# Kernel tuning notes

Hardware: AMD Instinct MI355X
Metric: run time of the kernel (lower is better)

## Reference

```python
import jax, jax.numpy as jnp
import numpy as np

B, L, D = 16, 1024, 512
EPS = 1e-6


def setup_inputs() -> dict:
    key = jax.random.key(0)
    ks = jax.random.split(key, 12)
    inp = {
        'q': jax.random.normal(ks[0], (B, L, D), jnp.float32),
        'k': jax.random.normal(ks[1], (B, L, D), jnp.float32),
        'v': jax.random.normal(ks[2], (B, L, D), jnp.float32),
        'inputs_lengths': jax.random.randint(ks[3], (B,), 1, L + 1),
        'distance_matrix': jax.random.uniform(ks[4], (B, L, L), jnp.float32),
        'Wq': jax.random.normal(ks[5], (D, D), jnp.float32) / np.sqrt(D),
        'Wk': jax.random.normal(ks[6], (D, D), jnp.float32) / np.sqrt(D),
        'Wv': jax.random.normal(ks[7], (D, D), jnp.float32) / np.sqrt(D),
        'Wqt': jax.random.normal(ks[8], (D, D), jnp.float32) / np.sqrt(D),
        'Wkt': jax.random.normal(ks[9], (D, D), jnp.float32) / np.sqrt(D),
        'Wfc': jax.random.normal(ks[10], (D, D), jnp.float32) / np.sqrt(D),
        'gamma': jnp.ones((D,), jnp.float32),
        'beta': jnp.zeros((D,), jnp.float32),
    }
    return inp


def reference(q, k, v, inputs_lengths, distance_matrix, Wq, Wk, Wv, Wqt, Wkt, Wfc, gamma, beta):
    temperature = jnp.asarray(D, q.dtype) ** 0.5
    residual = q
    # projections (torch Linear: x @ W.T)
    qp = jnp.einsum('bld,ed->ble', q, Wq)
    kp = jnp.einsum('bld,ed->ble', k, Wk)
    vp = jnp.einsum('bld,ed->ble', v, Wv)
    qt = jnp.einsum('bld,ed->ble', q, Wqt)
    kt = jnp.einsum('bld,ed->ble', k, Wkt)
    # distance-weighted time features: [B,L,L] @ [B,L,D]
    qt = jnp.einsum('blm,bmd->bld', distance_matrix, qt)
    kt = jnp.einsum('blm,bmd->bld', distance_matrix, kt)
    # scores: content + distance term
    attn = jnp.einsum('bld,bmd->blm', qp / temperature, kp)
    attn = attn + jnp.einsum('bld,bmd->blm', qt / temperature, kt)
    # pad_zero_masking: zero out key positions beyond each sequence length
    mask = (jnp.arange(L)[None, :] < inputs_lengths[:, None]).astype(attn.dtype)  # [B, L]
    mask = mask[:, None, :]  # [B, 1, L] broadcast over query dim
    attn = jnp.tanh(attn * mask) * mask
    out = jnp.einsum('blm,bmd->bld', attn, vp)
    out = jnp.einsum('bld,ed->ble', out, Wfc) + residual
    # LayerNorm(eps=1e-6)
    mu = jnp.mean(out, axis=-1, keepdims=True)
    var = jnp.mean((out - mu) ** 2, axis=-1, keepdims=True)
    out = (out - mu) * jax.lax.rsqrt(var + EPS) * gamma + beta
    return (out, attn)
```

## Files before the change

kernel.cpp:

```cpp
#include <hip/hip_runtime.h>
#include <math.h>

#define LL 1024
#define DD 512
#define NB 16

typedef __attribute__((ext_vector_type(8))) short bf16x8;
typedef __attribute__((ext_vector_type(4))) float f32x4;
typedef unsigned short u16;
typedef unsigned int u32;
typedef const __attribute__((address_space(1))) void* gptr_t;
typedef __attribute__((address_space(3))) void* sptr_t;

static const long NLD = (long)NB * LL * DD;
static const long NLL = (long)NB * LL * LL;

__device__ __forceinline__ u16 f2bf(float x) {
  u32 u = __float_as_uint(x);
  u += 0x7fffu + ((u >> 16) & 1u);
  return (u16)(u >> 16);
}
__device__ __forceinline__ float bf2f(u16 h) {
  return __uint_as_float((u32)h << 16);
}
// ... 60 lines not shown
    u16* __restrict__ Wq_h, u16* __restrict__ Wk_h, u16* __restrict__ Wv_h,
    u16* __restrict__ Wfc_h, u16* __restrict__ Wqt_h,
    u16* __restrict__ Wqt_l, u16* __restrict__ Wkt_h,
    u16* __restrict__ Wkt_l) {
  const int z = blockIdx.z;
  const float* x;
  u16 *hi, *lo = nullptr;
  switch (z) {
    case 0: x = Wq; hi = Wq_h; break;
    case 1: x = Wk; hi = Wk_h; break;
    case 2: x = Wv; hi = Wv_h; break;
    case 3: x = Wfc; hi = Wfc_h; break;
    case 4: x = Wqt; hi = Wqt_h; lo = Wqt_l; break;
    default: x = Wkt; hi = Wkt_h; lo = Wkt_l; break;
  }
  const long i = ((long)blockIdx.x * 256 + threadIdx.x) * 4;
  const float4 v = *(const float4*)(x + i);
  ushort4 h;
  h.x = f2bf(v.x);
  h.y = f2bf(v.y);
  h.z = f2bf(v.z);
  h.w = f2bf(v.w);
  *(ushort4*)(hi + i) = h;
  if (z >= 4) {
    ushort4 s;
    s.x = f2bf(v.x - bf2f(h.x));
    s.y = f2bf(v.y - bf2f(h.y));
    s.z = f2bf(v.z - bf2f(h.z));
    s.w = f2bf(v.w - bf2f(h.w));
    *(ushort4*)(lo + i) = s;
  }
}

template <int NISS>
__device__ __forceinline__ void stage_tile(const u16* __restrict__ G, long ld,
                                           int row0, int k0, char* lds, int w,
                                           int l) {
#pragma unroll
  for (int i = 0; i < NISS; ++i) {
    const int off = i * 4096 + w * 1024 + l * 16;
    const int r = off >> 6;
    const int cp = (off >> 4) & 3;
    const int c = cp ^ ((r >> 1) & 3);
    __builtin_amdgcn_global_load_lds(
        (gptr_t)(G + (long)(row0 + r) * ld + k0 + c * 8),
        (sptr_t)(lds + i * 4096 + w * 1024), 16, 0, 0);
  }
}

__device__ __forceinline__ bf16x8 read_frag(const char* lds, int r, int ks) {
  const int cp = ks ^ ((r >> 1) & 3);
  return *(const bf16x8*)(lds + r * 64 + cp * 16);
}

__device__ __forceinline__ void core_plain(const u16* __restrict__ A, long lda,
                                           const u16* __restrict__ B, long ldb,
                                           int K, int bm, int bn, char* smem,
                                           f32x4 acc[4][4]) {
  const int tid = threadIdx.x, w = tid >> 6, l = tid & 63;
  const int wm = (w >> 1) * 64, wn = (w & 1) * 64;
  const int fr = l & 15, ks = l >> 4;
  char* As = smem;
  char* Bs = smem + 8192;
  for (int k0 = 0; k0 < K; k0 += 32) {
    stage_tile<2>(A, lda, bm, k0, As, w, l);
    stage_tile<2>(B, ldb, bn, k0, Bs, w, l);
    __syncthreads();
    bf16x8 af[4], bg[4];
#pragma unroll
    for (int i = 0; i < 4; ++i) {
      af[i] = read_frag(As, wm + i * 16 + fr, ks);
      bg[i] = read_frag(Bs, wn + i * 16 + fr, ks);
    }
#pragma unroll
    for (int mi = 0; mi < 4; ++mi)
#pragma unroll
      for (int ni = 0; ni < 4; ++ni)
        acc[mi][ni] = __builtin_amdgcn_mfma_f32_16x16x32_bf16(
            af[mi], bg[ni], acc[mi][ni], 0, 0, 0);
    __syncthreads();
  }
}

__device__ __forceinline__ void core_split(
    const u16* __restrict__ Ah, const u16* __restrict__ Al, long lda,
    const u16* __restrict__ Bh, const u16* __restrict__ Bl, long ldb, int K,
    int bm, int bn, char* smem, f32x4 acc[4][4]) {
  const int tid = threadIdx.x, w = tid >> 6, l = tid & 63;
  const int wm = (w >> 1) * 64, wn = (w & 1) * 64;
  const int fr = l & 15, ks = l >> 4;
  char* Ash = smem;
  char* Bsh = smem + 8192;
  char* Asl = smem + 16384;
  char* Bsl = smem + 24576;
  for (int k0 = 0; k0 < K; k0 += 32) {
    stage_tile<2>(Ah, lda, bm, k0, Ash, w, l);
    stage_tile<2>(Bh, ldb, bn, k0, Bsh, w, l);
    stage_tile<2>(Al, lda, bm, k0, Asl, w, l);
    stage_tile<2>(Bl, ldb, bn, k0, Bsl, w, l);
    __syncthreads();
    bf16x8 ah[4], bh[4];
#pragma unroll
    for (int i = 0; i < 4; ++i) {
      ah[i] = read_frag(Ash, wm + i * 16 + fr, ks);
      bh[i] = read_frag(Bsh, wn + i * 16 + fr, ks);
    }
#pragma unroll
    for (int mi = 0; mi < 4; ++mi)
#pragma unroll
      for (int ni = 0; ni < 4; ++ni)
        acc[mi][ni] = __builtin_amdgcn_mfma_f32_16x16x32_bf16(
            ah[mi], bh[ni], acc[mi][ni], 0, 0, 0);
    bf16x8 bl[4];
#pragma unroll
    for (int ni = 0; ni < 4; ++ni)
      bl[ni] = read_frag(Bsl, wn + ni * 16 + fr, ks);
#pragma unroll
    for (int mi = 0; mi < 4; ++mi)
#pragma unroll
      for (int ni = 0; ni < 4; ++ni)
        acc[mi][ni] = __builtin_amdgcn_mfma_f32_16x16x32_bf16(
            ah[mi], bl[ni], acc[mi][ni], 0, 0, 0);
    bf16x8 al[4];
#pragma unroll
    for (int mi = 0; mi < 4; ++mi)
      al[mi] = read_frag(Asl, wm + mi * 16 + fr, ks);
#pragma unroll
    for (int mi = 0; mi < 4; ++mi)
#pragma unroll
      for (int ni = 0; ni < 4; ++ni)
        acc[mi][ni] = __builtin_amdgcn_mfma_f32_16x16x32_bf16(
            al[mi], bh[ni], acc[mi][ni], 0, 0, 0);
    __syncthreads();
  }
}

#define EPI_PROLOG()                                       \
  const int tid = threadIdx.x, w = tid >> 6, l = tid & 63; \
  const int wm = (w >> 1) * 64, wn = (w & 1) * 64;         \
  const int fr = l & 15, ks = l >> 4;

__device__ __forceinline__ int scan_batches(const int* __restrict__ lens,
                                            int e, int mult, int* loc,
                                            int* rem) {
  for (int i = 0; i < NB; ++i) {
    const int c = mult * ((lens[i] + 127) >> 7);
    if (e < c) {
      *loc = e;
      return i;
    }
    e -= c;
  }
  *rem = e;
  return -1;
}

__global__ __launch_bounds__(256, 3) void k_proj_p(
    const u16* __restrict__ q_hi, const u16* __restrict__ k_hi,
    const u16* __restrict__ v_hi, const u16* __restrict__ Wq_h,
    const u16* __restrict__ Wk_h, const u16* __restrict__ Wv_h,
    const int* __restrict__ lens, u16* __restrict__ qp, u16* __restrict__ kp,
    u16* __restrict__ vp) {
  const int flat = xcd_chunk16(blockIdx.x);
  const u16 *A, *B;
  u16* C;
  int bm, bn;
  if (flat < 512) {
    A = q_hi;
    B = Wq_h;
    C = qp;
    bm = (flat >> 2) * 128;
    bn = (flat & 3) * 128;
  } else {
    int loc, rem;
    int b = scan_batches(lens, flat - 512, 4, &loc, &rem);
    if (b >= 0) {
      A = k_hi;
      B = Wk_h;
      C = kp;
    } else {
      b = scan_batches(lens, rem, 4, &loc, &rem);
      if (b < 0) return;
      A = v_hi;
      B = Wv_h;
      C = vp;
    }
    bm = b * 1024 + (loc >> 2) * 128;
    bn = (loc & 3) * 128;
  }
  __shared__ __align__(16) char smem[16384];
  f32x4 acc[4][4] = {};
  core_plain(A, DD, B, DD, DD, bm, bn, smem, acc);
  EPI_PROLOG()
#pragma unroll
  for (int mi = 0; mi < 4; ++mi) {
    const int R0 = bm + wm + mi * 16 + ks * 4;
#pragma unroll
    for (int ni = 0; ni < 4; ++ni) {
      const int col = bn + wn + ni * 16 + fr;
#pragma unroll
      for (int j = 0; j < 4; ++j)
        C[(long)(R0 + j) * DD + col] = f2bf(acc[mi][ni][j]);
    }
  }
}

__global__ __launch_bounds__(256, 3) void k_proj_t(
    const u16* __restrict__ q_hi, const u16* __restrict__ q_lo,
    const u16* __restrict__ k_hi, const u16* __restrict__ k_lo,
    const u16* __restrict__ Wqt_h, const u16* __restrict__ Wqt_l,
    const u16* __restrict__ Wkt_h, const u16* __restrict__ Wkt_l,
    u16* __restrict__ qt0h, u16* __restrict__ qt0l, u16* __restrict__ kt0h,
    u16* __restrict__ kt0l) {
  const int sel = blockIdx.z;
  const u16* Ah = sel ? k_hi : q_hi;
  const u16* Al = sel ? k_lo : q_lo;
  const u16* Bh = sel ? Wkt_h : Wqt_h;
  const u16* Bl = sel ? Wkt_l : Wqt_l;
  u16* Ch = sel ? kt0h : qt0h;
  u16* Cl = sel ? kt0l : qt0l;
  __shared__ __align__(16) char smem[32768];
  const int bm = blockIdx.y * 128, bn = blockIdx.x * 128;
  f32x4 acc[4][4] = {};
  core_split(Ah, Al, DD, Bh, Bl, DD, DD, bm, bn, smem, acc);
  EPI_PROLOG()
#pragma unroll
  for (int mi = 0; mi < 4; ++mi) {
    const int R0 = bm + wm + mi * 16 + ks * 4;
#pragma unroll
    for (int ni = 0; ni < 4; ++ni) {
      const int col = bn + wn + ni * 16 + fr;
#pragma unroll
      for (int j = 0; j < 4; ++j) {
        const long idx = (long)(R0 + j) * DD + col;
        const float x = acc[mi][ni][j];
        const u16 h = f2bf(x);
        Ch[idx] = h;
        Cl[idx] = f2bf(x - bf2f(h));
      }
    }
  }
}

__global__ __launch_bounds__(256) void k_tr(
    const u16* __restrict__ qt0h, const u16* __restrict__ qt0l,
    const u16* __restrict__ kt0h, const u16* __restrict__ kt0l,
    const u16* __restrict__ vp, const int* __restrict__ lens,
    u16* __restrict__ qTh, u16* __restrict__ qTl, u16* __restrict__ kTh,
    u16* __restrict__ kTl, u16* __restrict__ vpT) {
  const int z = blockIdx.z;
  const int b = z / 5, s = z - b * 5;
  const int r0 = blockIdx.y * 64, c0 = blockIdx.x * 64;
  if (s == 4 && r0 >= lens[b]) return;
  const u16* X;
  u16* O;
  switch (s) {
    case 0: X = qt0h; O = qTh; break;
    case 1: X = qt0l; O = qTl; break;
    case 2: X = kt0h; O = kTh; break;
    case 3: X = kt0l; O = kTl; break;
    default: X = vp; O = vpT; break;
  }
  X += (long)b * LL * DD;
  O += (long)b * LL * DD;
  __shared__ u16 t[64][68];
  const int tid = threadIdx.x;
#pragma unroll
  for (int i = 0; i < 16; ++i) {
    const int idx = tid + i * 256;
    t[idx >> 6][idx & 63] = X[(long)(r0 + (idx >> 6)) * DD + c0 + (idx & 63)];
  }
  __syncthreads();
#pragma unroll
  for (int i = 0; i < 16; ++i) {
    const int idx = tid + i * 256;
    const int rr = idx >> 6, cc = idx & 63;
    O[(long)(c0 + rr) * LL + r0 + cc] = t[cc][rr];
  }
}

__global__ __launch_bounds__(256, 3) void k_dist_g(
    const u16* __restrict__ dist_h, const u16* __restrict__ dist_l,
    const u16* __restrict__ qT_h, const u16* __restrict__ qT_l,
    const u16* __restrict__ kT_h, const u16* __restrict__ kT_l,
    const int* __restrict__ lens, u16* __restrict__ qt_h,
    u16* __restrict__ qt_l, u16* __restrict__ kt_h, u16* __restrict__ kt_l) {
  const int flat = xcd_chunk16(blockIdx.x);
  int b, sel, bm, bn;
  if (flat < 512) {
    sel = 0;
    b = flat >> 5;
    const int r = flat & 31;
    const int s = r >> 4, inner = r & 15;
    bm = (s * 4 + (inner & 3)) * 128;
    bn = (inner >> 2) * 128;
  } else {
    int loc, rem;
    b = scan_batches(lens, flat - 512, 4, &loc, &rem);
    if (b < 0) return;
    sel = 1;
    bm = (loc >> 2) * 128;
    bn = (loc & 3) * 128;
  }
  const u16* Ah = dist_h + (long)b * LL * LL;
  const u16* Al = dist_l + (long)b * LL * LL;
  const u16* Bh = (sel ? kT_h : qT_h) + (long)b * LL * DD;
  const u16* Bl = (sel ? kT_l : qT_l) + (long)b * LL * DD;
  u16* Oh = (sel ? kt_h : qt_h) + (long)b * LL * DD;
  u16* Ol = (sel ? kt_l : qt_l) + (long)b * LL * DD;
  __shared__ __align__(16) char smem[32768];
  f32x4 acc[4][4] = {};
  core_split(Ah, Al, LL, Bh, Bl, LL, LL, bm, bn, smem, acc);
  EPI_PROLOG()
#pragma unroll
  for (int mi = 0; mi < 4; ++mi) {
    const int R0 = bm + wm + mi * 16 + ks * 4;
#pragma unroll
    for (int ni = 0; ni < 4; ++ni) {
      const int col = bn + wn + ni * 16 + fr;
#pragma unroll
      for (int j = 0; j < 4; ++j) {
        const long idx = (long)(R0 + j) * DD + col;
        const float x = acc[mi][ni][j];
        const u16 h = f2bf(x);
        Oh[idx] = h;
        Ol[idx] = f2bf(x - bf2f(h));
      }
    }
  }
}

__global__ __launch_bounds__(256, 3) void k_score(
    const u16* __restrict__ qp, const u16* __restrict__ kp,
    const u16* __restrict__ qt_h, const u16* __restrict__ qt_l,
    const u16* __restrict__ kt_h, const u16* __restrict__ kt_l,
    const int* __restrict__ lens, float* __restrict__ attnF,
    u16* __restrict__ attnB) {
  const int tid = threadIdx.x;
  int loc, rem;
  int b = scan_batches(lens, xcd_chunk16(blockIdx.x), 8, &loc, &rem);
  int bm, bn;
  if (b < 0) {
    for (int i = 0; i < NB; ++i) {
      const int nbn = (lens[i] + 127) >> 7;
      const int c = (8 - nbn) << 3;
      if (rem < c) {
        b = i;
        const int wdt = 8 - nbn;
        bm = (rem / wdt) * 128;
        bn = (nbn + rem % wdt) * 128;
        break;
      }
      rem -= c;
    }
    if (b < 0) return;
    const long baseF = (long)b * LL * LL;
    const float4 zf = make_float4(0.f, 0.f, 0.f, 0.f);
    const ushort4 zh = {0, 0, 0, 0};
    for (int i = tid; i < 4096; i += 256) {
      const int row = i >> 5, c = (i & 31) << 2;
      const long idx = baseF + (long)(bm + row) * LL + bn + c;
      *(float4*)&attnF[idx] = zf;
      *(ushort4*)&attnB[idx] = zh;
    }
    return;
  }
  const int nbn = (lens[b] + 127) >> 7;
  {
    const int S = nbn << 2;
    const int s = loc / S, inner = loc - s * S;
    bm = (s * 4 + (inner & 3)) * 128;
    bn = (inner >> 2) * 128;
  }
  const int len = lens[b];
  const long baseF = (long)b * LL * LL;
  const long od = (long)b * LL * DD;
  const u16* Ah = qt_h + od;
  const u16* Al = qt_l + od;
  const u16* Bh = kt_h + od;
  const u16* Bl = kt_l + od;
  const u16* Ap = qp + od;
  const u16* Bp = kp + od;
  __shared__ __align__(16) char smem[49152];
  char* Ash = smem;
  char* Bsh = smem + 8192;
  char* Asl = smem + 16384;
  char* Bsl = smem + 24576;
  char* Aps = smem + 32768;
  char* Bps = smem + 40960;
  const int w = tid >> 6, l = tid & 63;
  const int wm = (w >> 1) * 64, wn = (w & 1) * 64;
  const int fr = l & 15, ks = l >> 4;
  f32x4 acc[4][4] = {};
  for (int k0 = 0; k0 < DD; k0 += 32) {
    stage_tile<2>(Ah, DD, bm, k0, Ash, w, l);
    stage_tile<2>(Bh, DD, bn, k0, Bsh, w, l);
    stage_tile<2>(Al, DD, bm, k0, Asl, w, l);
    stage_tile<2>(Bl, DD, bn, k0, Bsl, w, l);
    stage_tile<2>(Ap, DD, bm, k0, Aps, w, l);
    stage_tile<2>(Bp, DD, bn, k0, Bps, w, l);
    __syncthreads();
    bf16x8 ah[4], bh[4];
#pragma unroll
    for (int i = 0; i < 4; ++i) {
      ah[i] = read_frag(Ash, wm + i * 16 + fr, ks);
      bh[i] = read_frag(Bsh, wn + i * 16 + fr, ks);
    }
#pragma unroll
    for (int mi = 0; mi < 4; ++mi)
#pragma unroll
      for (int ni = 0; ni < 4; ++ni)
        acc[mi][ni] = __builtin_amdgcn_mfma_f32_16x16x32_bf16(
            ah[mi], bh[ni], acc[mi][ni], 0, 0, 0);
    bf16x8 bl[4];
#pragma unroll
    for (int ni = 0; ni < 4; ++ni)
      bl[ni] = read_frag(Bsl, wn + ni * 16 + fr, ks);
#pragma unroll
    for (int mi = 0; mi < 4; ++mi)
#pragma unroll
      for (int ni = 0; ni < 4; ++ni)
        acc[mi][ni] = __builtin_amdgcn_mfma_f32_16x16x32_bf16(
            ah[mi], bl[ni], acc[mi][ni], 0, 0, 0);
    bf16x8 al[4];
#pragma unroll
    for (int mi = 0; mi < 4; ++mi)
      al[mi] = read_frag(Asl, wm + mi * 16 + fr, ks);
#pragma unroll
    for (int mi = 0; mi < 4; ++mi)
#pragma unroll
      for (int ni = 0; ni < 4; ++ni)
        acc[mi][ni] = __builtin_amdgcn_mfma_f32_16x16x32_bf16(
            al[mi], bh[ni], acc[mi][ni], 0, 0, 0);
    bf16x8 ap[4], bp[4];
#pragma unroll
    for (int i = 0; i < 4; ++i) {
      ap[i] = read_frag(Aps, wm + i * 16 + fr, ks);
      bp[i] = read_frag(Bps, wn + i * 16 + fr, ks);
    }
#pragma unroll
    for (int mi = 0; mi < 4; ++mi)
#pragma unroll
      for (int ni = 0; ni < 4; ++ni)
        acc[mi][ni] = __builtin_amdgcn_mfma_f32_16x16x32_bf16(
            ap[mi], bp[ni], acc[mi][ni], 0, 0, 0);
    __syncthreads();
  }
  const float invt = 0.04419417382415922f;
#pragma unroll
  for (int mi = 0; mi < 4; ++mi) {
    const int R0 = bm + wm + mi * 16 + ks * 4;
#pragma unroll
    for (int ni = 0; ni < 4; ++ni) {
      const int col = bn + wn + ni * 16 + fr;
      const float m = (col < len) ? 1.0f : 0.0f;
#pragma unroll
      for (int j = 0; j < 4; ++j) {
        const float s = tanhf(acc[mi][ni][j] * invt * m) * m;
        const long idx = baseF + (long)(R0 + j) * LL + col;
        attnF[idx] = s;
        attnB[idx] = f2bf(s);
      }
    }
  }
}

__global__ __launch_bounds__(256, 3) void k_pv(const u16* __restrict__ attnB,
                                               const u16* __restrict__ vpT,
                                               const int* __restrict__ lens,
                                               u16* __restrict__ out0) {
  const int flat = xcd_chunk16(blockIdx.x);
  const int b = flat >> 5;
  const int r = flat & 31;
  const int bm = (r >> 2) * 128, bn = (r & 3) * 128;
  const int Kt = ((lens[b] + 31) >> 5) << 5;
  __shared__ __align__(16) char smem[16384];
  f32x4 acc[4][4] = {};
  core_plain(attnB + (long)b * LL * LL, LL, vpT + (long)b * LL * DD, LL, Kt,
             bm, bn, smem, acc);
  u16* C = out0 + (long)b * LL * DD;
  EPI_PROLOG()
#pragma unroll
  for (int mi = 0; mi < 4; ++mi) {
    const int R0 = bm + wm + mi * 16 + ks * 4;
#pragma unroll
    for (int ni = 0; ni < 4; ++ni) {
      const int col = bn + wn + ni * 16 + fr;
#pragma unroll
      for (int j = 0; j < 4; ++j)
        C[(long)(R0 + j) * DD + col] = f2bf(acc[mi][ni][j]);
    }
  }
}

__global__ __launch_bounds__(256, 2) void k_fcln(
    const u16* __restrict__ out0, const u16* __restrict__ Wfc_h,
    const float* __restrict__ q, const float* __restrict__ gamma,
    const float* __restrict__ beta, float* __restrict__ outO) {
  __shared__ __align__(16) char smem[36864];
  __shared__ float red[2][64][5];
  const int tid = threadIdx.x, w = tid >> 6, l = tid & 63;
  const int wn = w * 128;
  const int fr = l & 15, ks = l >> 4;
  const int bm = blockIdx.x * 64;
  char* As = smem;
  char* Bs = smem + 4096;
  f32x4 acc[4][8] = {};
  for (int k0 = 0; k0 < DD; k0 += 32) {
    stage_tile<1>(out0, DD, bm, k0, As, w, l);
    stage_tile<8>(Wfc_h, DD, 0, k0, Bs, w, l);
    __syncthreads();
    bf16x8 af[4], bg[8];
#pragma unroll
    for (int mi = 0; mi < 4; ++mi) af[mi] = read_frag(As, mi * 16 + fr, ks);
#pragma unroll
    for (int ni = 0; ni < 8; ++ni)
      bg[ni] = read_frag(Bs, wn + ni * 16 + fr, ks);
#pragma unroll
    for (int mi = 0; mi < 4; ++mi)
#pragma unroll
      for (int ni = 0; ni < 8; ++ni)
        acc[mi][ni] = __builtin_amdgcn_mfma_f32_16x16x32_bf16(
            af[mi], bg[ni], acc[mi][ni], 0, 0, 0);
    __syncthreads();
  }
  float p1[4][4], p2[4][4];
#pragma unroll
  for (int mi = 0; mi < 4; ++mi)
#pragma unroll
    for (int j = 0; j < 4; ++j) {
      p1[mi][j] = 0.0f;
      p2[mi][j] = 0.0f;
    }
#pragma unroll
  for (int mi = 0; mi < 4; ++mi) {
    const int r = mi * 16 + ks * 4;
#pragma unroll
    for (int ni = 0; ni < 8; ++ni) {
      const int col = wn + ni * 16 + fr;
#pragma unroll
      for (int j = 0; j < 4; ++j) {
        const float val = acc[mi][ni][j] + q[(long)(bm + r + j) * DD + col];
        acc[mi][ni][j] = val;
        p1[mi][j] += val;
        p2[mi][j] += val * val;
      }
    }
  }
#pragma unroll
  for (int off = 1; off < 16; off <<= 1) {
#pragma unroll
    for (int mi = 0; mi < 4; ++mi)
#pragma unroll
      for (int j = 0; j < 4; ++j) {
        p1[mi][j] += __shfl_xor(p1[mi][j], off);
        p2[mi][j] += __shfl_xor(p2[mi][j], off);
      }
  }
  if (fr == 0) {
#pragma unroll
    for (int mi = 0; mi < 4; ++mi)
#pragma unroll
      for (int j = 0; j < 4; ++j) {
        red[0][mi * 16 + ks * 4 + j][w] = p1[mi][j];
        red[1][mi * 16 + ks * 4 + j][w] = p2[mi][j];
      }
  }
  __syncthreads();
#pragma unroll
  for (int mi = 0; mi < 4; ++mi) {
#pragma unroll
    for (int j = 0; j < 4; ++j) {
      const int r = mi * 16 + ks * 4 + j;
      const float s1 =
          red[0][r][0] + red[0][r][1] + red[0][r][2] + red[0][r][3];
      const float s2 =
          red[1][r][0] + red[1][r][1] + red[1][r][2] + red[1][r][3];
      const float mu = s1 * (1.0f / DD);
      const float rs = rsqrtf(s2 * (1.0f / DD) - mu * mu + 1e-6f);
#pragma unroll
      for (int ni = 0; ni < 8; ++ni) {
        const int col = wn + ni * 16 + fr;
        outO[(long)(bm + r) * DD + col] =
            (acc[mi][ni][j] - mu) * rs * gamma[col] + beta[col];
      }
    }
  }
}

extern "C" void kernel_launch(void* const* d_in, const int* in_sizes, int n_in,
                              void* d_out, int out_size, void* d_ws,
                              size_t ws_size, hipStream_t stream) {
  const float* q = (const float*)d_in[0];
  const float* k = (const float*)d_in[1];
  const float* v = (const float*)d_in[2];
  const int* lens = (const int*)d_in[3];
  const float* dist = (const float*)d_in[4];
  const float* Wq = (const float*)d_in[5];
  const float* Wk = (const float*)d_in[6];
  const float* Wv = (const float*)d_in[7];
  const float* Wqt = (const float*)d_in[8];
  const float* Wkt = (const float*)d_in[9];
  const float* Wfc = (const float*)d_in[10];
  const float* gamma = (const float*)d_in[11];
  const float* beta = (const float*)d_in[12];

  char* W = (char*)d_ws;
  const size_t SB = 16777216;
  u16* q_hi = (u16*)(W + 0 * SB);
  u16* q_lo = (u16*)(W + 1 * SB);
  u16* k_hi = (u16*)(W + 2 * SB);
  u16* k_lo = (u16*)(W + 3 * SB);
  u16* v_hi = (u16*)(W + 4 * SB);
  u16* dist_h = (u16*)(W + 5 * SB);
  u16* dist_l = (u16*)(W + 7 * SB);
  u16* qp_bf = (u16*)(W + 9 * SB);
  u16* kp_bf = (u16*)(W + 10 * SB);
  u16* vp_bf = (u16*)(W + 11 * SB);
  u16* qt0h = (u16*)(W + 12 * SB);
  u16* qt0l = (u16*)(W + 13 * SB);
  u16* kt0h = (u16*)(W + 14 * SB);
  u16* kt0l = (u16*)(W + 15 * SB);
  u16* qT_h = (u16*)(W + 16 * SB);
  u16* qT_l = (u16*)(W + 17 * SB);
  u16* kT_h = (u16*)(W + 18 * SB);
  u16* kT_l = (u16*)(W + 19 * SB);
  char* WB = W + 20 * SB;
  const size_t WS = 524288;
  u16* Wq_h = (u16*)(WB + 0 * WS);
  u16* Wk_h = (u16*)(WB + 1 * WS);
  u16* Wv_h = (u16*)(WB + 2 * WS);
  u16* Wfc_h = (u16*)(WB + 3 * WS);
  u16* Wqt_h = (u16*)(WB + 4 * WS);
  u16* Wqt_l = (u16*)(WB + 5 * WS);
  u16* Wkt_h = (u16*)(WB + 6 * WS);
  u16* Wkt_l = (u16*)(WB + 7 * WS);
  u16* qt_h = q_hi;
  u16* qt_l = q_lo;
  u16* kt_h = k_hi;
  u16* kt_l = k_lo;
  u16* vpT = v_hi;
  u16* attnB = dist_h;
  u16* out0 = qp_bf;

  float* outO = (float*)d_out;
  float* attnF = outO + NLD;

  dim3 blk(256);
  k_split3<<<dim3(1024, 1, 3), blk, 0, stream>>>(q, k, v, q_hi, q_lo, k_hi,
                                                 k_lo, v_hi);
  k_splitd<<<4096, blk, 0, stream>>>(dist, dist_h, dist_l);
  k_splitw<<<dim3(256, 1, 6), blk, 0, stream>>>(Wq, Wk, Wv, Wfc, Wqt, Wkt,
                                                Wq_h, Wk_h, Wv_h, Wfc_h,
                                                Wqt_h, Wqt_l, Wkt_h, Wkt_l);

  k_proj_p<<<1536, blk, 0, stream>>>(q_hi, k_hi, v_hi, Wq_h, Wk_h, Wv_h, lens,
                                     qp_bf, kp_bf, vp_bf);
  k_proj_t<<<dim3(4, 128, 2), blk, 0, stream>>>(q_hi, q_lo, k_hi, k_lo, Wqt_h,
                                                Wqt_l, Wkt_h, Wkt_l, qt0h,
                                                qt0l, kt0h, kt0l);
  k_tr<<<dim3(8, 16, 80), blk, 0, stream>>>(qt0h, qt0l, kt0h, kt0l, vp_bf,
                                            lens, qT_h, qT_l, kT_h, kT_l,
                                            vpT);
  k_dist_g<<<1024, blk, 0, stream>>>(dist_h, dist_l, qT_h, qT_l, kT_h, kT_l,
                                     lens, qt_h, qt_l, kt_h, kt_l);
  k_score<<<1024, blk, 0, stream>>>(qp_bf, kp_bf, qt_h, qt_l, kt_h, kt_l,
                                    lens, attnF, attnB);
  k_pv<<<512, blk, 0, stream>>>(attnB, vpT, lens, out0);
  k_fcln<<<256, blk, 0, stream>>>(out0, Wfc_h, q, gamma, beta, outO);
}
```

Measured before the change: 425.1 us.

## Widen split-GEMM tiles to 128x256 and fuse transposes into projection epilogues

Removes the separate transpose kernel by having the projection kernels write qt/kt hi/lo and vp directly in transposed layout. Widens the tiles of the split-precision GEMMs (proj_t, dist_g, score) from 128x128 to 128x256, doubling per-warp accumulators and raising LDS use to 48-72KB with dynamic shared memory. The aim is better operand reuse per staged A tile and one fewer kernel pass over memory. The cost is lower occupancy (launch bounds 2), fewer blocks, and strided transposed stores in the epilogues.

```diff
diff --git a/kernel.cpp b/kernel.cpp
--- a/kernel.cpp
+++ b/kernel.cpp
@@ -166,55 +166,56 @@
   }
 }
 
-__device__ __forceinline__ void core_split(
+__device__ __forceinline__ void core_split2(
     const u16* __restrict__ Ah, const u16* __restrict__ Al, long lda,
     const u16* __restrict__ Bh, const u16* __restrict__ Bl, long ldb, int K,
-    int bm, int bn, char* smem, f32x4 acc[4][4]) {
+    int bm, int bn, char* smem, f32x4 acc[4][8]) {
   const int tid = threadIdx.x, w = tid >> 6, l = tid & 63;
-  const int wm = (w >> 1) * 64, wn = (w & 1) * 64;
+  const int wm = (w >> 1) * 64, wn = (w & 1) * 128;
   const int fr = l & 15, ks = l >> 4;
   char* Ash = smem;
-  char* Bsh = smem + 8192;
-  char* Asl = smem + 16384;
-  char* Bsl = smem + 24576;
+  char* Asl = smem + 8192;
+  char* Bsh = smem + 16384;
+  char* Bsl = smem + 32768;
   for (int k0 = 0; k0 < K; k0 += 32) {
     stage_tile<2>(Ah, lda, bm, k0, Ash, w, l);
-    stage_tile<2>(Bh, ldb, bn, k0, Bsh, w, l);
     stage_tile<2>(Al, lda, bm, k0, Asl, w, l);
-    stage_tile<2>(Bl, ldb, bn, k0, Bsl, w, l);
+    stage_tile<4>(Bh, ldb, bn, k0, Bsh, w, l);
+    stage_tile<4>(Bl, ldb, bn, k0, Bsl, w, l);
     __syncthreads();
-    bf16x8 ah[4], bh[4];
-#pragma unroll
-    for (int i = 0; i < 4; ++i) {
-      ah[i] = read_frag(Ash, wm + i * 16 + fr, ks);
-      bh[i] = read_frag(Bsh, wn + i * 16 + fr, ks);
-    }
-#pragma unroll
-    for (int mi = 0; mi < 4; ++mi)
-#pragma unroll
-      for (int ni = 0; ni < 4; ++ni)
+    bf16x8 ah[4], bh[8];
+#pragma unroll
+    for (int mi = 0; mi < 4; ++mi)
+      ah[mi] = read_frag(Ash, wm + mi * 16 + fr, ks);
+#pragma unroll
+    for (int ni = 0; ni < 8; ++ni)
+      bh[ni] = read_frag(Bsh, wn + ni * 16 + fr, ks);
+#pragma unroll
+    for (int mi = 0; mi < 4; ++mi)
+#pragma unroll
+      for (int ni = 0; ni < 8; ++ni)
         acc[mi][ni] = __builtin_amdgcn_mfma_f32_16x16x32_bf16(
             ah[mi], bh[ni], acc[mi][ni], 0, 0, 0);
-    bf16x8 bl[4];
-#pragma unroll
-    for (int ni = 0; ni < 4; ++ni)
+    bf16x8 al[4];
+#pragma unroll
+    for (int mi = 0; mi < 4; ++mi)
+      al[mi] = read_frag(Asl, wm + mi * 16 + fr, ks);
+#pragma unroll
+    for (int mi = 0; mi < 4; ++mi)
+#pragma unroll
+      for (int ni = 0; ni < 8; ++ni)
+        acc[mi][ni] = __builtin_amdgcn_mfma_f32_16x16x32_bf16(
+            al[mi], bh[ni], acc[mi][ni], 0, 0, 0);
+    bf16x8 bl[8];
+#pragma unroll
+    for (int ni = 0; ni < 8; ++ni)
       bl[ni] = read_frag(Bsl, wn + ni * 16 + fr, ks);
 #pragma unroll
     for (int mi = 0; mi < 4; ++mi)
 #pragma unroll
-      for (int ni = 0; ni < 4; ++ni)
+      for (int ni = 0; ni < 8; ++ni)
         acc[mi][ni] = __builtin_amdgcn_mfma_f32_16x16x32_bf16(
             ah[mi], bl[ni], acc[mi][ni], 0, 0, 0);
-    bf16x8 al[4];
-#pragma unroll
-    for (int mi = 0; mi < 4; ++mi)
-      al[mi] = read_frag(Asl, wm + mi * 16 + fr, ks);
-#pragma unroll
-    for (int mi = 0; mi < 4; ++mi)
-#pragma unroll
-      for (int ni = 0; ni < 4; ++ni)
-        acc[mi][ni] = __builtin_amdgcn_mfma_f32_16x16x32_bf16(
-            al[mi], bh[ni], acc[mi][ni], 0, 0, 0);
     __syncthreads();
   }
 }
@@ -222,6 +223,11 @@
 #define EPI_PROLOG()                                       \
   const int tid = threadIdx.x, w = tid >> 6, l = tid & 63; \
   const int wm = (w >> 1) * 64, wn = (w & 1) * 64;         \
+  const int fr = l & 15, ks = l >> 4;
+
+#define EPI_PROLOG2()                                      \
+  const int tid = threadIdx.x, w = tid >> 6, l = tid & 63; \
+  const int wm = (w >> 1) * 64, wn = (w & 1) * 128;        \
   const int fr = l & 15, ks = l >> 4;
 
 __device__ __forceinline__ int scan_batches(const int* __restrict__ lens,
@@ -238,17 +244,32 @@
   *rem = e;
   return -1;
 }
+__device__ __forceinline__ int scan_batches256(const int* __restrict__ lens,
+                                               int e, int mult, int* loc,
+                                               int* rem) {
+  for (int i = 0; i < NB; ++i) {
+    const int c = mult * ((lens[i] + 255) >> 8);
+    if (e < c) {
+      *loc = e;
+      return i;
+    }
+    e -= c;
+  }
+  *rem = e;
+  return -1;
+}
 
 __global__ __launch_bounds__(256, 3) void k_proj_p(
     const u16* __restrict__ q_hi, const u16* __restrict__ k_hi,
     const u16* __restrict__ v_hi, const u16* __restrict__ Wq_h,
     const u16* __restrict__ Wk_h, const u16* __restrict__ Wv_h,
     const int* __restrict__ lens, u16* __restrict__ qp, u16* __restrict__ kp,
-    u16* __restrict__ vp) {
+    u16* __restrict__ vpT) {
   const int flat = xcd_chunk16(blockIdx.x);
   const u16 *A, *B;
   u16* C;
   int bm, bn;
+  bool isV = false;
   if (flat < 512) {
     A = q_hi;
     B = Wq_h;
@@ -267,7 +288,8 @@
       if (b < 0) return;
       A = v_hi;
       B = Wv_h;
-      C = vp;
+      C = vpT;
+      isV = true;
     }
     bm = b * 1024 + (loc >> 2) * 128;
     bn = (loc & 3) * 128;
@@ -282,88 +304,67 @@
 #pragma unroll
     for (int ni = 0; ni < 4; ++ni) {
       const int col = bn + wn + ni * 16 + fr;
-#pragma unroll
-      for (int j = 0; j < 4; ++j)
-        C[(long)(R0 + j) * DD + col] = f2bf(acc[mi][ni][j]);
-    }
-  }
-}
-
-__global__ __launch_bounds__(256, 3) void k_proj_t(
+      if (isV) {
+        const long base = (long)(R0 >> 10) * LL * DD + (long)col * LL + (R0 & 1023);
+        ushort4 hv;
+        hv.x = f2bf(acc[mi][ni][0]);
+        hv.y = f2bf(acc[mi][ni][1]);
+        hv.z = f2bf(acc[mi][ni][2]);
+        hv.w = f2bf(acc[mi][ni][3]);
+        *(ushort4*)&C[base] = hv;
+      } else {
+#pragma unroll
+        for (int j = 0; j < 4; ++j)
+          C[(long)(R0 + j) * DD + col] = f2bf(acc[mi][ni][j]);
+      }
+    }
+  }
+}
+
+__global__ __launch_bounds__(256, 2) void k_proj_t(
     const u16* __restrict__ q_hi, const u16* __restrict__ q_lo,
     const u16* __restrict__ k_hi, const u16* __restrict__ k_lo,
     const u16* __restrict__ Wqt_h, const u16* __restrict__ Wqt_l,
     const u16* __restrict__ Wkt_h, const u16* __restrict__ Wkt_l,
-    u16* __restrict__ qt0h, u16* __restrict__ qt0l, u16* __restrict__ kt0h,
-    u16* __restrict__ kt0l) {
-  const int sel = blockIdx.z;
+    u16* __restrict__ qT_h, u16* __restrict__ qT_l, u16* __restrict__ kT_h,
+    u16* __restrict__ kT_l) {
+  const int flat = xcd_chunk16(blockIdx.x);
+  const int sel = flat >> 8;
+  const int r = flat & 255;
+  const int bm = (r >> 1) * 128, bn = (r & 1) * 256;
   const u16* Ah = sel ? k_hi : q_hi;
   const u16* Al = sel ? k_lo : q_lo;
   const u16* Bh = sel ? Wkt_h : Wqt_h;
   const u16* Bl = sel ? Wkt_l : Wqt_l;
-  u16* Ch = sel ? kt0h : qt0h;
-  u16* Cl = sel ? kt0l : qt0l;
-  __shared__ __align__(16) char smem[32768];
-  const int bm = blockIdx.y * 128, bn = blockIdx.x * 128;
-  f32x4 acc[4][4] = {};
-  core_split(Ah, Al, DD, Bh, Bl, DD, DD, bm, bn, smem, acc);
-  EPI_PROLOG()
+  u16* Ch = sel ? kT_h : qT_h;
+  u16* Cl = sel ? kT_l : qT_l;
+  __shared__ __align__(16) char smem[49152];
+  f32x4 acc[4][8] = {};
+  core_split2(Ah, Al, DD, Bh, Bl, DD, DD, bm, bn, smem, acc);
+  EPI_PROLOG2()
 #pragma unroll
   for (int mi = 0; mi < 4; ++mi) {
     const int R0 = bm + wm + mi * 16 + ks * 4;
-#pragma unroll
-    for (int ni = 0; ni < 4; ++ni) {
+    const long tb = (long)(R0 >> 10) * LL * DD + (R0 & 1023);
+#pragma unroll
+    for (int ni = 0; ni < 8; ++ni) {
       const int col = bn + wn + ni * 16 + fr;
+      const long base = tb + (long)col * LL;
+      ushort4 hv, lv;
 #pragma unroll
       for (int j = 0; j < 4; ++j) {
-        const long idx = (long)(R0 + j) * DD + col;
         const float x = acc[mi][ni][j];
         const u16 h = f2bf(x);
-        Ch[idx] = h;
-        Cl[idx] = f2bf(x - bf2f(h));
-      }
-    }
-  }
-}
-
-__global__ __launch_bounds__(256) void k_tr(
-    const u16* __restrict__ qt0h, const u16* __restrict__ qt0l,
-    const u16* __restrict__ kt0h, const u16* __restrict__ kt0l,
-    const u16* __restrict__ vp, const int* __restrict__ lens,
-    u16* __restrict__ qTh, u16* __restrict__ qTl, u16* __restrict__ kTh,
-    u16* __restrict__ kTl, u16* __restrict__ vpT) {
-  const int z = blockIdx.z;
-  const int b = z / 5, s = z - b * 5;
-  const int r0 = blockIdx.y * 64, c0 = blockIdx.x * 64;
-  if (s == 4 && r0 >= lens[b]) return;
-  const u16* X;
-  u16* O;
-  switch (s) {
-    case 0: X = qt0h; O = qTh; break;
-    case 1: X = qt0l; O = qTl; break;
-    case 2: X = kt0h; O = kTh; break;
-    case 3: X = kt0l; O = kTl; break;
-    default: X = vp; O = vpT; break;
-  }
-  X += (long)b * LL * DD;
-  O += (long)b * LL * DD;
-  __shared__ u16 t[64][68];
-  const int tid = threadIdx.x;
-#pragma unroll
-  for (int i = 0; i < 16; ++i) {
-    const int idx = tid + i * 256;
-    t[idx >> 6][idx & 63] = X[(long)(r0 + (idx >> 6)) * DD + c0 + (idx & 63)];
-  }
-  __syncthreads();
-#pragma unroll
-  for (int i = 0; i < 16; ++i) {
-    const int idx = tid + i * 256;
-    const int rr = idx >> 6, cc = idx & 63;
-    O[(long)(c0 + rr) * LL + r0 + cc] = t[cc][rr];
-  }
-}
-
-__global__ __launch_bounds__(256, 3) void k_dist_g(
+        ((u16*)&hv)[j] = h;
+        ((u16*)&lv)[j] = f2bf(x - bf2f(h));
+      }
+      *(ushort4*)&Ch[base] = hv;
+      *(ushort4*)&Cl[base] = lv;
+    }
+  }
+}
+
+__global__ __launch_bounds__(256, 2) void k_dist_g(
     const u16* __restrict__ dist_h, const u16* __restrict__ dist_l,
     const u16* __restrict__ qT_h, const u16* __restrict__ qT_l,
     const u16* __restrict__ kT_h, const u16* __restrict__ kT_l,
@@ -371,20 +372,19 @@
     u16* __restrict__ qt_l, u16* __restrict__ kt_h, u16* __restrict__ kt_l) {
   const int flat = xcd_chunk16(blockIdx.x);
   int b, sel, bm, bn;
-  if (flat < 512) {
+  if (flat < 256) {
     sel = 0;
-    b = flat >> 5;
-    const int r = flat & 31;
-    const int s = r >> 4, inner = r & 15;
-    bm = (s * 4 + (inner & 3)) * 128;
-    bn = (inner >> 2) * 128;
+    b = flat & 15;
+    const int r = flat >> 4;
+    bm = (r >> 1) * 128;
+    bn = (r & 1) * 256;
   } else {
     int loc, rem;
-    b = scan_batches(lens, flat - 512, 4, &loc, &rem);
+    b = scan_batches(lens, flat - 256, 2, &loc, &rem);
     if (b < 0) return;
     sel = 1;
-    bm = (loc >> 2) * 128;
-    bn = (loc & 3) * 128;
+    bm = (loc >> 1) * 128;
+    bn = (loc & 1) * 256;
   }
   const u16* Ah = dist_h + (long)b * LL * LL;
   const u16* Al = dist_l + (long)b * LL * LL;
@@ -392,15 +392,15 @@
   const u16* Bl = (sel ? kT_l : qT_l) + (long)b * LL * DD;
   u16* Oh = (sel ? kt_h : qt_h) + (long)b * LL * DD;
   u16* Ol = (sel ? kt_l : qt_l) + (long)b * LL * DD;
-  __shared__ __align__(16) char smem[32768];
-  f32x4 acc[4][4] = {};
-  core_split(Ah, Al, LL, Bh, Bl, LL, LL, bm, bn, smem, acc);
-  EPI_PROLOG()
+  __shared__ __align__(16) char smem[49152];
+  f32x4 acc[4][8] = {};
+  core_split2(Ah, Al, LL, Bh, Bl, LL, LL, bm, bn, smem, acc);
+  EPI_PROLOG2()
 #pragma unroll
   for (int mi = 0; mi < 4; ++mi) {
     const int R0 = bm + wm + mi * 16 + ks * 4;
 #pragma unroll
-    for (int ni = 0; ni < 4; ++ni) {
+    for (int ni = 0; ni < 8; ++ni) {
       const int col = bn + wn + ni * 16 + fr;
 #pragma unroll
       for (int j = 0; j < 4; ++j) {
@@ -414,25 +414,26 @@
   }
 }
 
-__global__ __launch_bounds__(256, 3) void k_score(
+__global__ __launch_bounds__(256, 2) void k_score(
     const u16* __restrict__ qp, const u16* __restrict__ kp,
     const u16* __restrict__ qt_h, const u16* __restrict__ qt_l,
     const u16* __restrict__ kt_h, const u16* __restrict__ kt_l,
     const int* __restrict__ lens, float* __restrict__ attnF,
     u16* __restrict__ attnB) {
+  extern __shared__ __align__(16) char dsm[];
   const int tid = threadIdx.x;
   int loc, rem;
-  int b = scan_batches(lens, xcd_chunk16(blockIdx.x), 8, &loc, &rem);
+  int b = scan_batches256(lens, xcd_chunk16(blockIdx.x), 8, &loc, &rem);
   int bm, bn;
   if (b < 0) {
     for (int i = 0; i < NB; ++i) {
-      const int nbn = (lens[i] + 127) >> 7;
-      const int c = (8 - nbn) << 3;
+      const int nbn = (lens[i] + 255) >> 8;
+      const int wdt = 4 - nbn;
+      const int c = wdt << 3;
       if (rem < c) {
         b = i;
-        const int wdt = 8 - nbn;
         bm = (rem / wdt) * 128;
-        bn = (nbn + rem % wdt) * 128;
+        bn = (nbn + rem % wdt) * 256;
         break;
       }
       rem -= c;
@@ -441,20 +442,20 @@
     const long baseF = (long)b * LL * LL;
     const float4 zf = make_float4(0.f, 0.f, 0.f, 0.f);
     const ushort4 zh = {0, 0, 0, 0};
-    for (int i = tid; i < 4096; i += 256) {
-      const int row = i >> 5, c = (i & 31) << 2;
-      const long idx = baseF + (long)(bm + row) * LL + bn + c;
+    for (int i = tid; i < 8192; i += 256) {
+      const int row = i >> 6, c4 = (i & 63) << 2;
+      const long idx = baseF + (long)(bm + row) * LL + bn + c4;
       *(float4*)&attnF[idx] = zf;
       *(ushort4*)&attnB[idx] = zh;
     }
     return;
   }
-  const int nbn = (lens[b] + 127) >> 7;
+  const int nbn = (lens[b] + 255) >> 8;
   {
     const int S = nbn << 2;
     const int s = loc / S, inner = loc - s * S;
     bm = (s * 4 + (inner & 3)) * 128;
-    bn = (inner >> 2) * 128;
+    bn = (inner >> 2) * 256;
   }
   const int len = lens[b];
   const long baseF = (long)b * LL * LL;
@@ -465,67 +466,68 @@
   const u16* Bl = kt_l + od;
   const u16* Ap = qp + od;
   const u16* Bp = kp + od;
-  __shared__ __align__(16) char smem[49152];
-  char* Ash = smem;
-  char* Bsh = smem + 8192;
-  char* Asl = smem + 16384;
-  char* Bsl = smem + 24576;
-  char* Aps = smem + 32768;
-  char* Bps = smem + 40960;
+  char* Ash = dsm;
+  char* Asl = dsm + 8192;
+  char* Bsh = dsm + 16384;
+  char* Bsl = dsm + 32768;
+  char* Aps = dsm + 49152;
+  char* Bps = dsm + 57344;
   const int w = tid >> 6, l = tid & 63;
-  const int wm = (w >> 1) * 64, wn = (w & 1) * 64;
+  const int wm = (w >> 1) * 64, wn = (w & 1) * 128;
   const int fr = l & 15, ks = l >> 4;
-  f32x4 acc[4][4] = {};
+  f32x4 acc[4][8] = {};
   for (int k0 = 0; k0 < DD; k0 += 32) {
     stage_tile<2>(Ah, DD, bm, k0, Ash, w, l);
-    stage_tile<2>(Bh, DD, bn, k0, Bsh, w, l);
     stage_tile<2>(Al, DD, bm, k0, Asl, w, l);
-    stage_tile<2>(Bl, DD, bn, k0, Bsl, w, l);
+    stage_tile<4>(Bh, DD, bn, k0, Bsh, w, l);
+    stage_tile<4>(Bl, DD, bn, k0, Bsl, w, l);
     stage_tile<2>(Ap, DD, bm, k0, Aps, w, l);
-    stage_tile<2>(Bp, DD, bn, k0, Bps, w, l);
+    stage_tile<4>(Bp, DD, bn, k0, Bps, w, l);
     __syncthreads();
-    bf16x8 ah[4], bh[4];
-#pragma unroll
-    for (int i = 0; i < 4; ++i) {
-      ah[i] = read_frag(Ash, wm + i * 16 + fr, ks);
-      bh[i] = read_frag(Bsh, wn + i * 16 + fr, ks);
-    }
-#pragma unroll
-    for (int mi = 0; mi < 4; ++mi)
-#pragma unroll
-      for (int ni = 0; ni < 4; ++ni)
+    bf16x8 ah[4], bh[8];
+#pragma unroll
+    for (int mi = 0; mi < 4; ++mi)
+      ah[mi] = read_frag(Ash, wm + mi * 16 + fr, ks);
+#pragma unroll
+    for (int ni = 0; ni < 8; ++ni)
+      bh[ni] = read_frag(Bsh, wn + ni * 16 + fr, ks);
+#pragma unroll
+    for (int mi = 0; mi < 4; ++mi)
+#pragma unroll
+      for (int ni = 0; ni < 8; ++ni)
         acc[mi][ni] = __builtin_amdgcn_mfma_f32_16x16x32_bf16(
             ah[mi], bh[ni], acc[mi][ni], 0, 0, 0);
-    bf16x8 bl[4];
-#pragma unroll
-    for (int ni = 0; ni < 4; ++ni)
+    bf16x8 al[4];
+#pragma unroll
+    for (int mi = 0; mi < 4; ++mi)
+      al[mi] = read_frag(Asl, wm + mi * 16 + fr, ks);
+#pragma unroll
+    for (int mi = 0; mi < 4; ++mi)
+#pragma unroll
+      for (int ni = 0; ni < 8; ++ni)
+        acc[mi][ni] = __builtin_amdgcn_mfma_f32_16x16x32_bf16(
+            al[mi], bh[ni], acc[mi][ni], 0, 0, 0);
+    bf16x8 bl[8];
+#pragma unroll
+    for (int ni = 0; ni < 8; ++ni)
       bl[ni] = read_frag(Bsl, wn + ni * 16 + fr, ks);
 #pragma unroll
     for (int mi = 0; mi < 4; ++mi)
 #pragma unroll
-      for (int ni = 0; ni < 4; ++ni)
+      for (int ni = 0; ni < 8; ++ni)
         acc[mi][ni] = __builtin_amdgcn_mfma_f32_16x16x32_bf16(
             ah[mi], bl[ni], acc[mi][ni], 0, 0, 0);
-    bf16x8 al[4];
-#pragma unroll
-    for (int mi = 0; mi < 4; ++mi)
-      al[mi] = read_frag(Asl, wm + mi * 16 + fr, ks);
-#pragma unroll
-    for (int mi = 0; mi < 4; ++mi)
-#pragma unroll
-      for (int ni = 0; ni < 4; ++ni)
-        acc[mi][ni] = __builtin_amdgcn_mfma_f32_16x16x32_bf16(
-            al[mi], bh[ni], acc[mi][ni], 0, 0, 0);
-    bf16x8 ap[4], bp[4];
-#pragma unroll
-    for (int i = 0; i < 4; ++i) {
-      ap[i] = read_frag(Aps, wm + i * 16 + fr, ks);
-      bp[i] = read_frag(Bps, wn + i * 16 + fr, ks);
-    }
-#pragma unroll
-    for (int mi = 0; mi < 4; ++mi)
-#pragma unroll
-      for (int ni = 0; ni < 4; ++ni)
+    bf16x8 ap[4], bp[8];
+#pragma unroll
+    for (int mi = 0; mi < 4; ++mi)
+      ap[mi] = read_frag(Aps, wm + mi * 16 + fr, ks);
+#pragma unroll
+    for (int ni = 0; ni < 8; ++ni)
+      bp[ni] = read_frag(Bps, wn + ni * 16 + fr, ks);
+#pragma unroll
+    for (int mi = 0; mi < 4; ++mi)
+#pragma unroll
+      for (int ni = 0; ni < 8; ++ni)
         acc[mi][ni] = __builtin_amdgcn_mfma_f32_16x16x32_bf16(
             ap[mi], bp[ni], acc[mi][ni], 0, 0, 0);
     __syncthreads();
@@ -535,7 +537,7 @@
   for (int mi = 0; mi < 4; ++mi) {
     const int R0 = bm + wm + mi * 16 + ks * 4;
 #pragma unroll
-    for (int ni = 0; ni < 4; ++ni) {
+    for (int ni = 0; ni < 8; ++ni) {
       const int col = bn + wn + ni * 16 + fr;
       const float m = (col < len) ? 1.0f : 0.0f;
 #pragma unroll
@@ -689,6 +691,9 @@
   const float* gamma = (const float*)d_in[11];
   const float* beta = (const float*)d_in[12];
 
+  (void)hipFuncSetAttribute((const void*)k_score,
+                            hipFuncAttributeMaxDynamicSharedMemorySize, 73728);
+
   char* W = (char*)d_ws;
   const size_t SB = 16777216;
   u16* q_hi = (u16*)(W + 0 * SB);
@@ -700,11 +705,7 @@
   u16* dist_l = (u16*)(W + 7 * SB);
   u16* qp_bf = (u16*)(W + 9 * SB);
   u16* kp_bf = (u16*)(W + 10 * SB);
-  u16* vp_bf = (u16*)(W + 11 * SB);
-  u16* qt0h = (u16*)(W + 12 * SB);
-  u16* qt0l = (u16*)(W + 13 * SB);
-  u16* kt0h = (u16*)(W + 14 * SB);
-  u16* kt0l = (u16*)(W + 15 * SB);
+  u16* vpT = (u16*)(W + 11 * SB);
   u16* qT_h = (u16*)(W + 16 * SB);
   u16* qT_l = (u16*)(W + 17 * SB);
   u16* kT_h = (u16*)(W + 18 * SB);
@@ -723,7 +724,6 @@
   u16* qt_l = q_lo;
   u16* kt_h = k_hi;
   u16* kt_l = k_lo;
-  u16* vpT = v_hi;
   u16* attnB = dist_h;
   u16* out0 = qp_bf;
 
@@ -739,17 +739,13 @@
                                                 Wqt_h, Wqt_l, Wkt_h, Wkt_l);
 
   k_proj_p<<<1536, blk, 0, stream>>>(q_hi, k_hi, v_hi, Wq_h, Wk_h, Wv_h, lens,
-                                     qp_bf, kp_bf, vp_bf);
-  k_proj_t<<<dim3(4, 128, 2), blk, 0, stream>>>(q_hi, q_lo, k_hi, k_lo, Wqt_h,
-                                                Wqt_l, Wkt_h, Wkt_l, qt0h,
-                                                qt0l, kt0h, kt0l);
-  k_tr<<<dim3(8, 16, 80), blk, 0, stream>>>(qt0h, qt0l, kt0h, kt0l, vp_bf,
-                                            lens, qT_h, qT_l, kT_h, kT_l,
-                                            vpT);
-  k_dist_g<<<1024, blk, 0, stream>>>(dist_h, dist_l, qT_h, qT_l, kT_h, kT_l,
-                                     lens, qt_h, qt_l, kt_h, kt_l);
-  k_score<<<1024, blk, 0, stream>>>(qp_bf, kp_bf, qt_h, qt_l, kt_h, kt_l,
-                                    lens, attnF, attnB);
+                                     qp_bf, kp_bf, vpT);
+  k_proj_t<<<512, blk, 0, stream>>>(q_hi, q_lo, k_hi, k_lo, Wqt_h, Wqt_l,
+                                    Wkt_h, Wkt_l, qT_h, qT_l, kT_h, kT_l);
+  k_dist_g<<<512, blk, 0, stream>>>(dist_h, dist_l, qT_h, qT_l, kT_h, kT_l,
+                                    lens, qt_h, qt_l, kt_h, kt_l);
+  k_score<<<512, blk, 73728, stream>>>(qp_bf, kp_bf, qt_h, qt_l, kt_h, kt_l,
+                                       lens, attnF, attnB);
   k_pv<<<512, blk, 0, stream>>>(attnB, vpT, lens, out0);
   k_fcln<<<256, blk, 0, stream>>>(out0, Wfc_h, q, gamma, beta, outO);
 }
```

Measured after the change: 506.7 us. 1.19x slower.

## Fuse transpose into projection epilogues and drop separate transpose kernel

Applied to the files above, without the earlier changes.

The V projection and the time-feature projections now write their outputs already transposed, staged through shared memory with vectorized stores. This removes the standalone transpose kernel and the round trip of the intermediate buffers through global memory. In exchange, the epilogues gain extra syncs and shared-memory use: a new 16 KB buffer in the plain projection kernel, and reuse of the staging buffer in the split one. This may reduce occupancy for k_proj_p.

```diff
diff --git a/kernel.cpp b/kernel.cpp
--- a/kernel.cpp
+++ b/kernel.cpp
@@ -244,11 +244,12 @@
     const u16* __restrict__ v_hi, const u16* __restrict__ Wq_h,
     const u16* __restrict__ Wk_h, const u16* __restrict__ Wv_h,
     const int* __restrict__ lens, u16* __restrict__ qp, u16* __restrict__ kp,
-    u16* __restrict__ vp) {
+    u16* __restrict__ vpT) {
   const int flat = xcd_chunk16(blockIdx.x);
   const u16 *A, *B;
   u16* C;
   int bm, bn;
+  bool isV = false;
   if (flat < 512) {
     A = q_hi;
     B = Wq_h;
@@ -267,24 +268,55 @@
       if (b < 0) return;
       A = v_hi;
       B = Wv_h;
-      C = vp;
+      C = vpT;
+      isV = true;
     }
     bm = b * 1024 + (loc >> 2) * 128;
     bn = (loc & 3) * 128;
   }
   __shared__ __align__(16) char smem[16384];
+  __shared__ __align__(16) u16 tb[64 * 132];
   f32x4 acc[4][4] = {};
   core_plain(A, DD, B, DD, DD, bm, bn, smem, acc);
   EPI_PROLOG()
-#pragma unroll
-  for (int mi = 0; mi < 4; ++mi) {
-    const int R0 = bm + wm + mi * 16 + ks * 4;
-#pragma unroll
-    for (int ni = 0; ni < 4; ++ni) {
-      const int col = bn + wn + ni * 16 + fr;
-#pragma unroll
-      for (int j = 0; j < 4; ++j)
-        C[(long)(R0 + j) * DD + col] = f2bf(acc[mi][ni][j]);
+  if (isV) {
+    const int b = bm >> 10, lr0 = bm & 1023;
+    for (int half = 0; half < 2; ++half) {
+      __syncthreads();
+      if ((wn >> 6) == half) {
+#pragma unroll
+        for (int mi = 0; mi < 4; ++mi) {
+          const int rloc = wm + mi * 16 + ks * 4;
+#pragma unroll
+          for (int ni = 0; ni < 4; ++ni) {
+            const int cloc = ni * 16 + fr;
+#pragma unroll
+            for (int j = 0; j < 4; ++j)
+              tb[cloc * 132 + rloc + j] = f2bf(acc[mi][ni][j]);
+          }
+        }
+      }
+      __syncthreads();
+      const int colg0 = bn + half * 64;
+#pragma unroll
+      for (int it = 0; it < 8; ++it) {
+        const int i = (it * 256 + tid) * 4;
+        const int cl = i >> 7, rl = i & 127;
+        *(ushort4*)&C[(long)b * LL * DD + (long)(colg0 + cl) * LL + lr0 + rl] =
+            *(ushort4*)&tb[cl * 132 + rl];
+      }
+    }
+  } else {
+#pragma unroll
+    for (int mi = 0; mi < 4; ++mi) {
+      const int R0 = bm + wm + mi * 16 + ks * 4;
+#pragma unroll
+      for (int ni = 0; ni < 4; ++ni) {
+        const int col = bn + wn + ni * 16 + fr;
+#pragma unroll
+        for (int j = 0; j < 4; ++j)
+          C[(long)(R0 + j) * DD + col] = f2bf(acc[mi][ni][j]);
+      }
     }
   }
 }
@@ -294,72 +326,52 @@
     const u16* __restrict__ k_hi, const u16* __restrict__ k_lo,
     const u16* __restrict__ Wqt_h, const u16* __restrict__ Wqt_l,
     const u16* __restrict__ Wkt_h, const u16* __restrict__ Wkt_l,
-    u16* __restrict__ qt0h, u16* __restrict__ qt0l, u16* __restrict__ kt0h,
-    u16* __restrict__ kt0l) {
+    u16* __restrict__ qT_h, u16* __restrict__ qT_l, u16* __restrict__ kT_h,
+    u16* __restrict__ kT_l) {
   const int sel = blockIdx.z;
   const u16* Ah = sel ? k_hi : q_hi;
   const u16* Al = sel ? k_lo : q_lo;
   const u16* Bh = sel ? Wkt_h : Wqt_h;
   const u16* Bl = sel ? Wkt_l : Wqt_l;
-  u16* Ch = sel ? kt0h : qt0h;
-  u16* Cl = sel ? kt0l : qt0l;
+  u16* Ch = sel ? kT_h : qT_h;
+  u16* Cl = sel ? kT_l : qT_l;
   __shared__ __align__(16) char smem[32768];
   const int bm = blockIdx.y * 128, bn = blockIdx.x * 128;
   f32x4 acc[4][4] = {};
   core_split(Ah, Al, DD, Bh, Bl, DD, DD, bm, bn, smem, acc);
   EPI_PROLOG()
-#pragma unroll
-  for (int mi = 0; mi < 4; ++mi) {
-    const int R0 = bm + wm + mi * 16 + ks * 4;
-#pragma unroll
-    for (int ni = 0; ni < 4; ++ni) {
-      const int col = bn + wn + ni * 16 + fr;
-#pragma unroll
-      for (int j = 0; j < 4; ++j) {
-        const long idx = (long)(R0 + j) * DD + col;
-        const float x = acc[mi][ni][j];
-        const u16 h = f2bf(x);
-        Ch[idx] = h;
-        Cl[idx] = f2bf(x - bf2f(h));
-      }
-    }
-  }
-}
-
-__global__ __launch_bounds__(256) void k_tr(
-    const u16* __restrict__ qt0h, const u16* __restrict__ qt0l,
-    const u16* __restrict__ kt0h, const u16* __restrict__ kt0l,
-    const u16* __restrict__ vp, const int* __restrict__ lens,
-    u16* __restrict__ qTh, u16* __restrict__ qTl, u16* __restrict__ kTh,
-    u16* __restrict__ kTl, u16* __restrict__ vpT) {
-  const int z = blockIdx.z;
-  const int b = z / 5, s = z - b * 5;
-  const int r0 = blockIdx.y * 64, c0 = blockIdx.x * 64;
-  if (s == 4 && r0 >= lens[b]) return;
-  const u16* X;
-  u16* O;
-  switch (s) {
-    case 0: X = qt0h; O = qTh; break;
-    case 1: X = qt0l; O = qTl; break;
-    case 2: X = kt0h; O = kTh; break;
-    case 3: X = kt0l; O = kTl; break;
-    default: X = vp; O = vpT; break;
-  }
-  X += (long)b * LL * DD;
-  O += (long)b * LL * DD;
-  __shared__ u16 t[64][68];
-  const int tid = threadIdx.x;
-#pragma unroll
-  for (int i = 0; i < 16; ++i) {
-    const int idx = tid + i * 256;
-    t[idx >> 6][idx & 63] = X[(long)(r0 + (idx >> 6)) * DD + c0 + (idx & 63)];
-  }
-  __syncthreads();
-#pragma unroll
-  for (int i = 0; i < 16; ++i) {
-    const int idx = tid + i * 256;
-    const int rr = idx >> 6, cc = idx & 63;
-    O[(long)(c0 + rr) * LL + r0 + cc] = t[cc][rr];
+  u16* tb = (u16*)smem;
+  const int b = bm >> 10, lr0 = bm & 1023;
+  for (int part = 0; part < 2; ++part) {
+    u16* OT = part ? Cl : Ch;
+    for (int half = 0; half < 2; ++half) {
+      __syncthreads();
+      if ((wn >> 6) == half) {
+#pragma unroll
+        for (int mi = 0; mi < 4; ++mi) {
+          const int rloc = wm + mi * 16 + ks * 4;
+#pragma unroll
+          for (int ni = 0; ni < 4; ++ni) {
+            const int cloc = ni * 16 + fr;
+#pragma unroll
+            for (int j = 0; j < 4; ++j) {
+              const float x = acc[mi][ni][j];
+              const u16 h = f2bf(x);
+              tb[cloc * 132 + rloc + j] = part ? f2bf(x - bf2f(h)) : h;
+            }
+          }
+        }
+      }
+      __syncthreads();
+      const int colg0 = bn + half * 64;
+#pragma unroll
+      for (int it = 0; it < 8; ++it) {
+        const int i = (it * 256 + tid) * 4;
+        const int cl = i >> 7, rl = i & 127;
+        *(ushort4*)&OT[(long)b * LL * DD + (long)(colg0 + cl) * LL + lr0 +
+                       rl] = *(ushort4*)&tb[cl * 132 + rl];
+      }
+    }
   }
 }
 
@@ -695,16 +707,12 @@
   u16* q_lo = (u16*)(W + 1 * SB);
   u16* k_hi = (u16*)(W + 2 * SB);
   u16* k_lo = (u16*)(W + 3 * SB);
-  u16* v_hi = (u16*)(W + 4 * SB);
   u16* dist_h = (u16*)(W + 5 * SB);
   u16* dist_l = (u16*)(W + 7 * SB);
   u16* qp_bf = (u16*)(W + 9 * SB);
   u16* kp_bf = (u16*)(W + 10 * SB);
-  u16* vp_bf = (u16*)(W + 11 * SB);
-  u16* qt0h = (u16*)(W + 12 * SB);
-  u16* qt0l = (u16*)(W + 13 * SB);
-  u16* kt0h = (u16*)(W + 14 * SB);
-  u16* kt0l = (u16*)(W + 15 * SB);
+  u16* vpT = (u16*)(W + 11 * SB);
+  u16* v_hi = (u16*)(W + 4 * SB);
   u16* qT_h = (u16*)(W + 16 * SB);
   u16* qT_l = (u16*)(W + 17 * SB);
   u16* kT_h = (u16*)(W + 18 * SB);
@@ -723,7 +731,6 @@
   u16* qt_l = q_lo;
   u16* kt_h = k_hi;
   u16* kt_l = k_lo;
-  u16* vpT = v_hi;
   u16* attnB = dist_h;
   u16* out0 = qp_bf;
 
@@ -739,13 +746,10 @@
                                                 Wqt_h, Wqt_l, Wkt_h, Wkt_l);
 
   k_proj_p<<<1536, blk, 0, stream>>>(q_hi, k_hi, v_hi, Wq_h, Wk_h, Wv_h, lens,
-                                     qp_bf, kp_bf, vp_bf);
+                                     qp_bf, kp_bf, vpT);
   k_proj_t<<<dim3(4, 128, 2), blk, 0, stream>>>(q_hi, q_lo, k_hi, k_lo, Wqt_h,
-                                                Wqt_l, Wkt_h, Wkt_l, qt0h,
-                                                qt0l, kt0h, kt0l);
-  k_tr<<<dim3(8, 16, 80), blk, 0, stream>>>(qt0h, qt0l, kt0h, kt0l, vp_bf,
-                                            lens, qT_h, qT_l, kT_h, kT_l,
-                                            vpT);
+                                                Wqt_l, Wkt_h, Wkt_l, qT_h,
+                                                qT_l, kT_h, kT_l);
   k_dist_g<<<1024, blk, 0, stream>>>(dist_h, dist_l, qT_h, qT_l, kT_h, kT_l,
                                      lens, qt_h, qt_l, kt_h, kt_l);
   k_score<<<1024, blk, 0, stream>>>(qp_bf, kp_bf, qt_h, qt_l, kt_h, kt_l,
```

Result: slower. 629.1 us (+48.0%).
